# Kernel optimization log

Measured on AMD Instinct MI355X. Metric: run time of the kernel, lower is better.

## Reference

```python
import jax, jax.numpy as jnp
import numpy as np

WS = 14            # window height/width
CLS = 1            # cls tokens
DIM = 768
H = 12             # heads
DH = DIM // H      # head dim = 64
B = 128
N = WS * WS + CLS  # 197
SCALE = DH ** (-0.5)
TABLE = (2 * WS - 1) ** 2 + CLS  # 730


def _rel_index():
    # Swin-style relative position index, with CLS rows/cols pointing at the
    # last table entry (torch uses index -1 which wraps to TABLE-1).
    c = np.arange(WS)
    coords = np.stack(np.meshgrid(c, c, indexing='ij'))      # [2,14,14]
    cf = coords.reshape(2, -1)                                # [2,196]
    rel = cf[:, :, None] - cf[:, None, :]                     # [2,196,196]
    rel = rel.transpose(1, 2, 0).astype(np.int64)             # [196,196,2]
    rel[..., 0] += WS - 1
    rel[..., 1] += WS - 1
    rel[..., 0] *= 2 * WS - 1
    idx = rel.sum(-1)                                         # [196,196]
    full = np.full((N, N), -1, np.int64)
    full[CLS:, CLS:] = idx
    full = np.where(full < 0, TABLE - 1, full)
    return jnp.asarray(full, jnp.int32)


def setup_inputs() -> dict:
    key = jax.random.key(0)
    ks = jax.random.split(key, 5)
    return {
        'x': jax.random.normal(ks[0], (B, N, DIM), jnp.float32),
        'qkv_w': jax.random.normal(ks[1], (3 * DIM, DIM), jnp.float32) * 0.02,
        'proj_w': jax.random.normal(ks[2], (DIM, DIM), jnp.float32) * 0.02,
        'proj_b': jnp.zeros((DIM,), jnp.float32),
        'bias_table': jax.random.normal(ks[3], (TABLE, H), jnp.float32) * 0.02,
        'rel_idx': _rel_index(),
    }


def reference(x, qkv_w, proj_w, proj_b, bias_table, rel_idx):
    Bc, Nc, C = x.shape
    qkv = x @ qkv_w.T                                   # [B,N,3C]
    qkv = qkv.reshape(Bc, Nc, 3, H, DH).transpose(2, 0, 3, 1, 4)
    q, k, v = qkv[0], qkv[1], qkv[2]                    # [B,H,N,D]
    attn = jnp.einsum('bhnd,bhmd->bhnm', q, k) * SCALE  # [B,H,N,N]
    bias = bias_table[rel_idx]                          # [N,N,H]
    attn = attn + bias.transpose(2, 0, 1)[None]         # broadcast over batch
    attn = jax.nn.softmax(attn, axis=-1)
    out = jnp.einsum('bhnm,bhmd->bhnd', attn, v)        # [B,H,N,D]
    out = out.transpose(0, 2, 1, 3).reshape(Bc, Nc, C)
    return out @ proj_w.T + proj_b
```

## Files before the change

### kernel.cpp

```cpp
#include <hip/hip_runtime.h>
#include <hip/hip_bf16.h>

typedef _Float16 half8 __attribute__((ext_vector_type(8)));
typedef _Float16 half4 __attribute__((ext_vector_type(4)));
typedef float floatx4 __attribute__((ext_vector_type(4)));

#define MFMA16(a, b, c) __builtin_amdgcn_mfma_f32_16x16x32_f16(a, b, c, 0, 0, 0)
#define GLDS16(gp, lp) __builtin_amdgcn_global_load_lds( \
    (const __attribute__((address_space(1))) void*)(gp), \
    (__attribute__((address_space(3))) void*)(lp), 16, 0, 0)

#define BATCH 128
#define NTOK 197
#define NPAD 208
#define DIM 768
#define NH 12
#define DH 64
#define M_ROWS (BATCH * NTOK)
#define MP_ROWS (BATCH * NPAD)
#define KPAD 224
#define NKT 13
#define NTILES (BATCH * NH * NKT)

#define PREP_X (MP_ROWS * (DIM / 8))
#define PREP_WQ (3 * DIM * DIM / 8)
#define PREP_WP (DIM * DIM / 8)
#define PREP_B (NH * 13 * 13 * 256)
#define PREP_TOT (PREP_X + PREP_WQ + PREP_WP + PREP_B)

__device__ __forceinline__ half8 cvt8(const float* s) {
    float4 v0 = *(const float4*)s;
    float4 v1 = *(const float4*)(s + 4);
    half8 o;
    o[0] = (_Float16)v0.x; o[1] = (_Float16)v0.y;
    o[2] = (_Float16)v0.z; o[3] = (_Float16)v0.w;
    o[4] = (_Float16)v1.x; o[5] = (_Float16)v1.y;
    o[6] = (_Float16)v1.z; o[7] = (_Float16)v1.w;
    return o;
}

__global__ void prep_kernel(const float* __restrict__ x,
                            const float* __restrict__ qkv_w,
                            const float* __restrict__ proj_w,
                            const float* __restrict__ table,
                            const int* __restrict__ ridx,
                            _Float16* __restrict__ xh,
                            _Float16* __restrict__ wqkvh,
                            _Float16* __restrict__ wprojh,
                            _Float16* __restrict__ biasph) {
    int idx = blockIdx.x * 256 + threadIdx.x;
    if (idx < PREP_X) {
        int row = idx / (DIM / 8), ch = idx - row * (DIM / 8);
        int b = row / NPAD, n = row - b * NPAD;
        half8 o = {};
        if (n < NTOK) o = cvt8(x + (size_t)(b * NTOK + n) * DIM + ch * 8);
        *(half8*)&xh[(size_t)row * DIM + ch * 8] = o;
        return;
    }
    idx -= PREP_X;
    if (idx < PREP_WQ) {
        *(half8*)&wqkvh[idx * 8] = cvt8(qkv_w + idx * 8);
        return;
    }
    idx -= PREP_WQ;
    if (idx < PREP_WP) {
        *(half8*)&wprojh[idx * 8] = cvt8(proj_w + idx * 8);
        return;
    }
    idx -= PREP_WP;
    if (idx < PREP_B) {
        int e = idx & 255;
        int r = e >> 4, q = (e >> 2) & 3, rr = e & 3;
        int t = idx >> 8;
        int nt = t % 13; int t2 = t / 13; int qt = t2 % 13; int h = t2 / 13;
        int row = qt * 16 + q * 4 + rr;
        int col = nt * 16 + r;
        float v = -30000.0f;
        if (col < NTOK) {
            int rc = row < NTOK ? row : NTOK - 1;
            v = table[ridx[rc * NTOK + col] * NH + h];
        }
        biasph[idx] = (_Float16)v;
    }
}

__device__ __forceinline__ void gemm_core_768(const _Float16* __restrict__ A,
                                              const _Float16* __restrict__ B,
                                              int m0b, int n0b,
                                              _Float16* As, _Float16* Bs,
                                              floatx4 acc[4][4]) {
    const int lane = threadIdx.x & 63;
    const int w = threadIdx.x >> 6;
    const int r = lane & 15, q = lane >> 4;
    const int mo = (w & 1) * 64;
    const int no = (w >> 1) * 64;
    const int srow = w * 32 + (lane >> 3);
    const int gatom = (lane & 7) ^ (lane >> 3);
    const int rx = r & 7;

    const _Float16* pa[4];
    const _Float16* pb[4];
#pragma unroll
    for (int c = 0; c < 4; ++c) {
        pa[c] = A + (size_t)(m0b + srow + c * 8) * DIM + gatom * 8;
        pb[c] = B + (size_t)(n0b + srow + c * 8) * DIM + gatom * 8;
    }
    _Float16* ldsA = As + w * 2048;
    _Float16* ldsB = Bs + w * 2048;

    for (int kk = 0; kk < DIM / 64; ++kk) {
#pragma unroll
        for (int c = 0; c < 4; ++c) {
            GLDS16(pa[c], ldsA + c * 512);
            GLDS16(pb[c], ldsB + c * 512);
            pa[c] += 64;
            pb[c] += 64;
        }
        __syncthreads();
#pragma unroll
        for (int s = 0; s < 2; ++s) {
            half8 a[4], b[4];
#pragma unroll
            for (int i = 0; i < 4; ++i)
                a[i] = *(const half8*)&As[((mo + i * 16 + r) * 8 + ((s * 4 + q) ^ rx)) * 8];
#pragma unroll
            for (int j = 0; j < 4; ++j)
                b[j] = *(const half8*)&Bs[((no + j * 16 + r) * 8 + ((s * 4 + q) ^ rx)) * 8];
#pragma unroll
            for (int i = 0; i < 4; ++i)
#pragma unroll
                for (int j = 0; j < 4; ++j)
                    acc[i][j] = MFMA16(a[i], b[j], acc[i][j]);
        }
        __syncthreads();
    }
}

__global__ __launch_bounds__(256) void qkv_gemm(const _Float16* __restrict__ X,
                                                const _Float16* __restrict__ W,
                                                _Float16* __restrict__ qh,
                                                _Float16* __restrict__ kh,
                                                _Float16* __restrict__ vt) {
    __shared__ __align__(16) _Float16 smem[17408];
    _Float16* As = smem;
    _Float16* Bs = smem + 8192;
    const int lane = threadIdx.x & 63;
    const int w = threadIdx.x >> 6;
    const int r = lane & 15, q = lane >> 4;

    const int id = blockIdx.x;
    const int xcd = id & 7;
    const int lid = id >> 3;
    const int bx = lid % 18;
    const int by = xcd * 26 + lid / 18;
    const int m0b = by * 128;
    const int n0b = bx * 128;

    floatx4 acc[4][4] = {};
    gemm_core_768(X, W, m0b, n0b, As, Bs, acc);

    const int which = n0b / 768;
    const int gw = (w & 1) * 64;
    const int cw = (w >> 1) * 64;
    _Float16* T = smem;

    if (which == 2) {
#pragma unroll
        for (int i = 0; i < 4; ++i) {
#pragma unroll
            for (int j = 0; j < 4; ++j) {
                half4 hv;
#pragma unroll
                for (int rr = 0; rr < 4; ++rr) hv[rr] = (_Float16)acc[i][j][rr];
                *(half4*)&T[(cw + j * 16 + r) * 136 + gw + i * 16 + q * 4] = hv;
            }
        }
    } else {
        const float scale = (which == 0) ? 0.125f : 1.0f;
#pragma unroll
        for (int i = 0; i < 4; ++i)
#pragma unroll
            for (int j = 0; j < 4; ++j)
#pragma unroll
                for (int rr = 0; rr < 4; ++rr)
                    T[(gw + i * 16 + q * 4 + rr) * 136 + cw + j * 16 + r] =
                        (_Float16)(acc[i][j][rr] * scale);
    }
    __syncthreads();

    const int t = threadIdx.x;
    if (which == 2) {
#pragma unroll
        for (int p = 0; p < 8; ++p) {
            int idx = p * 256 + t;
            int c = idx >> 4, g0 = (idx & 15) * 8;
            int grow = m0b + g0;
            int b_idx = grow / NPAD, n_idx = grow - b_idx * NPAD;
            int vcol = n0b + c - 1536;
            int hh = vcol >> 6, d = vcol & 63;
            half8 hv = *(const half8*)&T[c * 136 + g0];
            *(half8*)&vt[((size_t)(b_idx * NH + hh) * DH + d) * KPAD + n_idx] = hv;
        }
    } else {
        _Float16* dst = (which == 0) ? qh : kh;
#pragma unroll
        for (int p = 0; p < 8; ++p) {
            int idx = p * 256 + t;
            int g = idx >> 4, c0 = (idx & 15) * 8;
            int grow = m0b + g;
            int b_idx = grow / NPAD, n_idx = grow - b_idx * NPAD;
            int colm = (n0b + c0) % 768;
            int hh = colm >> 6, d0 = colm & 63;
            half8 hv = *(const half8*)&T[g * 136 + c0];
            *(half8*)&dst[((size_t)(b_idx * NH + hh) * NPAD + n_idx) * DH + d0] = hv;
        }
    }
}

__global__ __launch_bounds__(256) void proj_gemm(const _Float16* __restrict__ A,
                                                 const _Float16* __restrict__ W,
                                                 const float* __restrict__ bias,
                                                 float* __restrict__ out) {
    __shared__ __align__(16) _Float16 As[128 * 64];
    __shared__ __align__(16) _Float16 Bs[128 * 64];
    const int lane = threadIdx.x & 63;
    const int w = threadIdx.x >> 6;
    const int r = lane & 15, q = lane >> 4;

    const int id = blockIdx.x;
    const int xcd = id & 7;
    const int lid = id >> 3;
    const int bx = lid % 6;
    const int by = xcd * 25 + lid / 6;
    if (by >= 197) return;
    const int m0b = by * 128;
    const int n0b = bx * 128;

    floatx4 acc[4][4] = {};
    gemm_core_768(A, W, m0b, n0b, As, Bs, acc);

    const int m0 = m0b + (w & 1) * 64;
    const int n0 = n0b + (w >> 1) * 64;
#pragma unroll
    for (int i = 0; i < 4; ++i) {
#pragma unroll
        for (int rr = 0; rr < 4; ++rr) {
            size_t grow = m0 + i * 16 + q * 4 + rr;
#pragma unroll
            for (int j = 0; j < 4; ++j) {
                int gcol = n0 + j * 16 + r;
                out[grow * DIM + gcol] = acc[i][j][rr] + bias[gcol];
            }
        }
    }
}

__global__ __launch_bounds__(256) void attn_kernel(const _Float16* __restrict__ qh,
                                                   const _Float16* __restrict__ kh,
                                                   const _Float16* __restrict__ vt,
                                                   const _Float16* __restrict__ biasph,
                                                   _Float16* __restrict__ ah) {
    __shared__ __align__(16) _Float16 P[4][16][40];
    const int w = threadIdx.x >> 6, lane = threadIdx.x & 63;
    const int r = lane & 15, q = lane >> 4;
    const int T = blockIdx.x * 4 + w;
    const int bh = T / 13;
    const int qt = T - bh * 13;
    const int b = bh / NH, h = bh - b * NH;
    const _Float16* Qb = qh + (size_t)bh * NPAD * DH;
    const _Float16* Kb = kh + (size_t)bh * NPAD * DH;
    const _Float16* Vtb = vt + (size_t)bh * DH * KPAD;

    half4 bf[NKT];
    const _Float16* bbase = biasph + (((size_t)h * 13 + qt) * 13) * 256 + r * 16 + q * 4;
#pragma unroll
    for (int nt = 0; nt < NKT; ++nt)
        bf[nt] = *(const half4*)(bbase + nt * 256);

    const int rowq = qt * 16 + r;
    half8 aq0 = *(const half8*)(Qb + (size_t)rowq * DH + q * 8);
    half8 aq1 = *(const half8*)(Qb + (size_t)rowq * DH + 32 + q * 8);

    floatx4 sacc[NKT] = {};
#pragma unroll
    for (int nt = 0; nt < NKT; ++nt) {
        int rowk = nt * 16 + r;
        half8 b0 = *(const half8*)(Kb + (size_t)rowk * DH + q * 8);
        half8 b1 = *(const half8*)(Kb + (size_t)rowk * DH + 32 + q * 8);
        sacc[nt] = MFMA16(aq0, b0, sacc[nt]);
        sacc[nt] = MFMA16(aq1, b1, sacc[nt]);
    }

    _Float16 pv[NKT][4];
#pragma unroll
    for (int rr = 0; rr < 4; ++rr) {
        float sv[NKT];
        float sm = 0.f;
#pragma unroll
        for (int nt = 0; nt < NKT; ++nt) {
            float e = __expf(sacc[nt][rr] + (float)bf[nt][rr]);
            sv[nt] = e;
            sm += e;
        }
#pragma unroll
        for (int m = 1; m <= 8; m <<= 1) sm += __shfl_xor(sm, m, 64);
        float inv = 1.0f / sm;
#pragma unroll
        for (int nt = 0; nt < NKT; ++nt)
            pv[nt][rr] = (_Float16)(sv[nt] * inv);
    }

    floatx4 oacc[4] = {};
    _Float16* Pw = &P[w][0][0];
#pragma unroll
    for (int kt = 0; kt < 7; ++kt) {
        const int nt0 = kt * 2, nt1 = kt * 2 + 1;
#pragma unroll
        for (int rr = 0; rr < 4; ++rr) {
            Pw[(q * 4 + rr) * 40 + r] = pv[nt0][rr];
            Pw[(q * 4 + rr) * 40 + 16 + r] = (nt1 < NKT) ? pv[nt1][rr] : (_Float16)0.0f;
        }
        __asm__ volatile("" ::: "memory");
        half8 ap = *(const half8*)&Pw[r * 40 + q * 8];
        __asm__ volatile("" ::: "memory");
#pragma unroll
        for (int dt = 0; dt < 4; ++dt) {
            half8 bv = *(const half8*)(Vtb + (size_t)(dt * 16 + r) * KPAD + kt * 32 + q * 8);
            oacc[dt] = MFMA16(ap, bv, oacc[dt]);
        }
    }

#pragma unroll
    for (int rr = 0; rr < 4; ++rr) {
        int row = qt * 16 + q * 4 + rr;
        if (row < NTOK) {
            size_t o = ((size_t)b * NTOK + row) * DIM + h * DH;
#pragma unroll
            for (int dt = 0; dt < 4; ++dt)
                ah[o + dt * 16 + r] = (_Float16)oacc[dt][rr];
        }
    }
}

extern "C" void kernel_launch(void* const* d_in, const int* in_sizes, int n_in,
                              void* d_out, int out_size, void* d_ws, size_t ws_size,
                              hipStream_t stream) {
    const float* x = (const float*)d_in[0];
    const float* qkv_w = (const float*)d_in[1];
    const float* proj_w = (const float*)d_in[2];
    const float* proj_b = (const float*)d_in[3];
    const float* table = (const float*)d_in[4];
    const int* ridx = (const int*)d_in[5];
    float* out = (float*)d_out;

    char* ws = (char*)d_ws;
    const size_t SZ_XP = (size_t)MP_ROWS * DIM * 2;
    const size_t SZ_WQKV = (size_t)3 * DIM * DIM * 2;
    const size_t SZ_WPROJ = (size_t)DIM * DIM * 2;
    const size_t SZ_QK = (size_t)BATCH * NH * NPAD * DH * 2;
    const size_t SZ_VT = (size_t)BATCH * NH * DH * KPAD * 2;
    const size_t SZ_BIAS = (size_t)NH * 13 * 13 * 256 * 2;

    _Float16* xh = (_Float16*)(ws + 0);
    _Float16* ah = (_Float16*)(ws + 0);
    _Float16* wqkvh = (_Float16*)(ws + SZ_XP);
    _Float16* wprojh = (_Float16*)(ws + SZ_XP + SZ_WQKV);
    _Float16* qh = (_Float16*)(ws + SZ_XP + SZ_WQKV + SZ_WPROJ);
    _Float16* kh = (_Float16*)(ws + SZ_XP + SZ_WQKV + SZ_WPROJ + SZ_QK);
    _Float16* vt = (_Float16*)(ws + SZ_XP + SZ_WQKV + SZ_WPROJ + 2 * SZ_QK);
    _Float16* biasph = (_Float16*)(ws + SZ_XP + SZ_WQKV + SZ_WPROJ + 2 * SZ_QK + SZ_VT);
    (void)SZ_BIAS; (void)ws_size; (void)n_in; (void)in_sizes; (void)out_size;

    prep_kernel<<<(PREP_TOT + 255) / 256, 256, 0, stream>>>(
        x, qkv_w, proj_w, table, ridx, xh, wqkvh, wprojh, biasph);
    qkv_gemm<<<3744, 256, 0, stream>>>(xh, wqkvh, qh, kh, vt);
    attn_kernel<<<NTILES / 4, 256, 0, stream>>>(qh, kh, vt, biasph, ah);
    proj_gemm<<<1200, 256, 0, stream>>>(ah, wprojh, proj_b, out);
}
```

Measured before the change: 427.3 us.

## Replace QKV GEMM with 256x256 eight-wave pipelined kernel using direct-to-LDS loads

The 128x128 four-wave QKV GEMM is replaced by a 256x256 tile kernel with 8 waves, double-buffered LDS filled through global_load_lds, and interleaved barriers with setprio around MFMA phases. The aim is to raise arithmetic intensity per tile and overlap global loads with MFMA work. The epilogue now writes each half-tile through LDS in turn. The attention kernel also gets an XCD-aware block remap for cache locality. The larger tile brings heavy register and LDS use and hand-written waitcnt/barrier logic that is fragile.

```diff
diff --git a/kernel.cpp b/kernel.cpp
--- a/kernel.cpp
+++ b/kernel.cpp
@@ -27,6 +27,14 @@
 #define PREP_WP (DIM * DIM / 8)
 #define PREP_B (NH * 13 * 13 * 256)
 #define PREP_TOT (PREP_X + PREP_WQ + PREP_WP + PREP_B)
+
+#define BAR() __asm__ volatile("s_barrier" ::: "memory")
+#define VMW4() __asm__ volatile("s_waitcnt vmcnt(4)" ::: "memory")
+#define VMW0() __asm__ volatile("s_waitcnt vmcnt(0)" ::: "memory")
+
+#define STG(gp, lp) do { \
+    GLDS16((gp), (lp)); \
+    GLDS16((gp) + 64 * DIM, (lp) + 4096); } while (0)
 
 __device__ __forceinline__ half8 cvt8(const float* s) {
     float4 v0 = *(const float4*)s;
@@ -84,6 +92,206 @@
     }
 }
 
+template <int VM, bool STA, bool STB>
+__device__ __forceinline__ void qkv_tile(int t, _Float16* smem,
+                                         const _Float16* ga0, const _Float16* ga1,
+                                         const _Float16* gb0, const _Float16* gb1,
+                                         int sbase, int r, int q, int wm, int wn,
+                                         floatx4 (&acc)[8][4]) {
+    const int buf = t & 1;
+    const int r7 = r & 7;
+    const int sl0 = (q ^ r7) * 8;
+    const int sl1 = sl0 ^ 32;
+    _Float16* base = smem + buf * 32768;
+    const _Float16* Ab = base + wm * 8192 + r * 64;
+    const _Float16* Bb = base + 16384 + (wn >> 1) * 8192 + ((wn & 1) * 64 + r) * 64;
+    _Float16* sA0 = smem + (buf ^ 1) * 32768 + sbase;
+    _Float16* sA1 = sA0 + 8192;
+    _Float16* sB0 = base + 16384 + sbase;
+    _Float16* sB1 = sB0 + 8192;
+    const int kof1 = (t + 1) * 64, kof2 = (t + 2) * 64;
+
+    half8 a[4][2], b[4][2];
+
+#pragma unroll
+    for (int i = 0; i < 4; ++i) {
+        a[i][0] = *(const half8*)(Ab + i * 1024 + sl0);
+        a[i][1] = *(const half8*)(Ab + i * 1024 + sl1);
+    }
+#pragma unroll
+    for (int j = 0; j < 2; ++j) {
+        b[j][0] = *(const half8*)(Bb + j * 1024 + sl0);
+        b[j][1] = *(const half8*)(Bb + j * 1024 + sl1);
+    }
+    if (STA) STG(ga0 + kof1, sA0);
+    BAR();
+    __builtin_amdgcn_s_setprio(1);
+#pragma unroll
+    for (int s = 0; s < 2; ++s)
+#pragma unroll
+        for (int i = 0; i < 4; ++i)
+#pragma unroll
+            for (int j = 0; j < 2; ++j)
+                acc[i][j] = MFMA16(a[i][s], b[j][s], acc[i][j]);
+    __builtin_amdgcn_s_setprio(0);
+    BAR();
+
+#pragma unroll
+    for (int j = 0; j < 2; ++j) {
+        b[2 + j][0] = *(const half8*)(Bb + (2 + j) * 1024 + sl0);
+        b[2 + j][1] = *(const half8*)(Bb + (2 + j) * 1024 + sl1);
+    }
+    if (STA) STG(ga1 + kof1, sA1);
+    BAR();
+    __builtin_amdgcn_s_setprio(1);
+#pragma unroll
+    for (int s = 0; s < 2; ++s)
+#pragma unroll
+        for (int i = 0; i < 4; ++i)
+#pragma unroll
+            for (int j = 0; j < 2; ++j)
+                acc[i][2 + j] = MFMA16(a[i][s], b[2 + j][s], acc[i][2 + j]);
+    __builtin_amdgcn_s_setprio(0);
+    BAR();
+
+#pragma unroll
+    for (int i = 0; i < 4; ++i) {
+        a[i][0] = *(const half8*)(Ab + (4 + i) * 1024 + sl0);
+        a[i][1] = *(const half8*)(Ab + (4 + i) * 1024 + sl1);
+    }
+    if (STB) STG(gb0 + kof2, sB0);
+    BAR();
+    __builtin_amdgcn_s_setprio(1);
+#pragma unroll
+    for (int s = 0; s < 2; ++s)
+#pragma unroll
+        for (int i = 0; i < 4; ++i)
+#pragma unroll
+            for (int j = 0; j < 2; ++j)
+                acc[4 + i][j] = MFMA16(a[i][s], b[j][s], acc[4 + i][j]);
+    __builtin_amdgcn_s_setprio(0);
+    BAR();
+
+    if (STB) STG(gb1 + kof2, sB1);
+    BAR();
+    __builtin_amdgcn_s_setprio(1);
+#pragma unroll
+    for (int s = 0; s < 2; ++s)
+#pragma unroll
+        for (int i = 0; i < 4; ++i)
+#pragma unroll
+            for (int j = 0; j < 2; ++j)
+                acc[4 + i][2 + j] = MFMA16(a[i][s], b[2 + j][s], acc[4 + i][2 + j]);
+    __builtin_amdgcn_s_setprio(0);
+    if (VM == 4) { VMW4(); }
+    else if (VM == 0) { VMW0(); }
+    BAR();
+}
+
+__global__ __launch_bounds__(512, 2) void qkv_gemm8(const _Float16* __restrict__ X,
+                                                    const _Float16* __restrict__ W,
+                                                    _Float16* __restrict__ qh,
+                                                    _Float16* __restrict__ kh,
+                                                    _Float16* __restrict__ vt) {
+    __shared__ __align__(16) _Float16 smem[65536];
+    const int tid = threadIdx.x;
+    const int lane = tid & 63, wid = tid >> 6;
+    const int r = lane & 15, q = lane >> 4;
+    const int wm = wid >> 2, wn = wid & 3;
+
+    const int id = blockIdx.x;
+    const int swz = (id & 7) * 117 + (id >> 3);
+    const int by = swz / 9, bx = swz - by * 9;
+    const int m0b = by * 256, n0b = bx * 256;
+
+    const int srow = wid * 8 + (lane >> 3);
+    const int sch = (lane & 7) ^ (lane >> 3);
+    const _Float16* ga0 = X + (size_t)(m0b + srow) * DIM + sch * 8;
+    const _Float16* ga1 = ga0 + (size_t)128 * DIM;
+    const _Float16* gb0 = W + (size_t)(n0b + srow) * DIM + sch * 8;
+    const _Float16* gb1 = gb0 + (size_t)128 * DIM;
+    const int sbase = wid * 512;
+
+    floatx4 acc[8][4] = {};
+
+    STG(ga0, smem + sbase);
+    STG(ga1, smem + 8192 + sbase);
+    STG(gb0, smem + 16384 + sbase);
+    STG(gb1, smem + 24576 + sbase);
+    STG(gb0 + 64, smem + 32768 + 16384 + sbase);
+    STG(gb1 + 64, smem + 32768 + 24576 + sbase);
+    VMW4();
+    BAR();
+
+#pragma unroll 2
+    for (int t = 0; t < 10; ++t)
+        qkv_tile<4, true, true>(t, smem, ga0, ga1, gb0, gb1, sbase, r, q, wm, wn, acc);
+    qkv_tile<0, true, false>(10, smem, ga0, ga1, gb0, gb1, sbase, r, q, wm, wn, acc);
+    qkv_tile<2, false, false>(11, smem, ga0, ga1, gb0, gb1, sbase, r, q, wm, wn, acc);
+
+    __syncthreads();
+    const int which = bx / 3;
+    const int cb = (bx - which * 3) * 256;
+    if (which == 2) {
+#pragma unroll
+        for (int hp = 0; hp < 2; ++hp) {
+            if (wm == hp) {
+#pragma unroll
+                for (int i = 0; i < 8; ++i)
+#pragma unroll
+                    for (int j = 0; j < 4; ++j) {
+                        half4 hv;
+#pragma unroll
+                        for (int rr = 0; rr < 4; ++rr) hv[rr] = (_Float16)acc[i][j][rr];
+                        *(half4*)&smem[(wn * 64 + j * 16 + r) * 136 + i * 16 + q * 4] = hv;
+                    }
+            }
+            __syncthreads();
+#pragma unroll
+            for (int p = 0; p < 8; ++p) {
+                int idx = p * 512 + tid;
+                int c = idx >> 4, g0 = (idx & 15) * 8;
+                int grow = m0b + hp * 128 + g0;
+                int b_idx = grow / NPAD, n_idx = grow - b_idx * NPAD;
+                int vcol = cb + c;
+                int hh = vcol >> 6, d = vcol & 63;
+                half8 hv = *(const half8*)&smem[c * 136 + g0];
+                *(half8*)&vt[((size_t)(b_idx * NH + hh) * DH + d) * KPAD + n_idx] = hv;
+            }
+            __syncthreads();
+        }
+    } else {
+        const float scale = (which == 0) ? 0.125f : 1.0f;
+        _Float16* dst = (which == 0) ? qh : kh;
+#pragma unroll
+        for (int hp = 0; hp < 2; ++hp) {
+            if (wm == hp) {
+#pragma unroll
+                for (int i = 0; i < 8; ++i)
+#pragma unroll
+                    for (int j = 0; j < 4; ++j)
+#pragma unroll
+                        for (int rr = 0; rr < 4; ++rr)
+                            smem[(i * 16 + q * 4 + rr) * 272 + wn * 64 + j * 16 + r] =
+                                (_Float16)(acc[i][j][rr] * scale);
+            }
+            __syncthreads();
+#pragma unroll
+            for (int p = 0; p < 8; ++p) {
+                int idx = p * 512 + tid;
+                int g = idx >> 5, c0 = (idx & 31) * 8;
+                int grow = m0b + hp * 128 + g;
+                int b_idx = grow / NPAD, n_idx = grow - b_idx * NPAD;
+                int colm = cb + c0;
+                int hh = colm >> 6, d0 = colm & 63;
+                half8 hv = *(const half8*)&smem[g * 272 + c0];
+                *(half8*)&dst[((size_t)(b_idx * NH + hh) * NPAD + n_idx) * DH + d0] = hv;
+            }
+            __syncthreads();
+        }
+    }
+}
+
 __device__ __forceinline__ void gemm_core_768(const _Float16* __restrict__ A,
                                               const _Float16* __restrict__ B,
                                               int m0b, int n0b,
@@ -136,87 +344,6 @@
     }
 }
 
-__global__ __launch_bounds__(256) void qkv_gemm(const _Float16* __restrict__ X,
-                                                const _Float16* __restrict__ W,
-                                                _Float16* __restrict__ qh,
-                                                _Float16* __restrict__ kh,
-                                                _Float16* __restrict__ vt) {
-    __shared__ __align__(16) _Float16 smem[17408];
-    _Float16* As = smem;
-    _Float16* Bs = smem + 8192;
-    const int lane = threadIdx.x & 63;
-    const int w = threadIdx.x >> 6;
-    const int r = lane & 15, q = lane >> 4;
-
-    const int id = blockIdx.x;
-    const int xcd = id & 7;
-    const int lid = id >> 3;
-    const int bx = lid % 18;
-    const int by = xcd * 26 + lid / 18;
-    const int m0b = by * 128;
-    const int n0b = bx * 128;
-
-    floatx4 acc[4][4] = {};
-    gemm_core_768(X, W, m0b, n0b, As, Bs, acc);
-
-    const int which = n0b / 768;
-    const int gw = (w & 1) * 64;
-    const int cw = (w >> 1) * 64;
-    _Float16* T = smem;
-
-    if (which == 2) {
-#pragma unroll
-        for (int i = 0; i < 4; ++i) {
-#pragma unroll
-            for (int j = 0; j < 4; ++j) {
-                half4 hv;
-#pragma unroll
-                for (int rr = 0; rr < 4; ++rr) hv[rr] = (_Float16)acc[i][j][rr];
-                *(half4*)&T[(cw + j * 16 + r) * 136 + gw + i * 16 + q * 4] = hv;
-            }
-        }
-    } else {
-        const float scale = (which == 0) ? 0.125f : 1.0f;
-#pragma unroll
-        for (int i = 0; i < 4; ++i)
-#pragma unroll
-            for (int j = 0; j < 4; ++j)
-#pragma unroll
-                for (int rr = 0; rr < 4; ++rr)
-                    T[(gw + i * 16 + q * 4 + rr) * 136 + cw + j * 16 + r] =
-                        (_Float16)(acc[i][j][rr] * scale);
-    }
-    __syncthreads();
-
-    const int t = threadIdx.x;
-    if (which == 2) {
-#pragma unroll
-        for (int p = 0; p < 8; ++p) {
-            int idx = p * 256 + t;
-            int c = idx >> 4, g0 = (idx & 15) * 8;
-            int grow = m0b + g0;
-            int b_idx = grow / NPAD, n_idx = grow - b_idx * NPAD;
-            int vcol = n0b + c - 1536;
-            int hh = vcol >> 6, d = vcol & 63;
-            half8 hv = *(const half8*)&T[c * 136 + g0];
-            *(half8*)&vt[((size_t)(b_idx * NH + hh) * DH + d) * KPAD + n_idx] = hv;
-        }
-    } else {
-        _Float16* dst = (which == 0) ? qh : kh;
-#pragma unroll
-        for (int p = 0; p < 8; ++p) {
-            int idx = p * 256 + t;
-            int g = idx >> 4, c0 = (idx & 15) * 8;
-            int grow = m0b + g;
-            int b_idx = grow / NPAD, n_idx = grow - b_idx * NPAD;
-            int colm = (n0b + c0) % 768;
-            int hh = colm >> 6, d0 = colm & 63;
-            half8 hv = *(const half8*)&T[g * 136 + c0];
-            *(half8*)&dst[((size_t)(b_idx * NH + hh) * NPAD + n_idx) * DH + d0] = hv;
-        }
-    }
-}
-
 __global__ __launch_bounds__(256) void proj_gemm(const _Float16* __restrict__ A,
                                                  const _Float16* __restrict__ W,
                                                  const float* __restrict__ bias,
@@ -263,7 +390,9 @@
     __shared__ __align__(16) _Float16 P[4][16][40];
     const int w = threadIdx.x >> 6, lane = threadIdx.x & 63;
     const int r = lane & 15, q = lane >> 4;
-    const int T = blockIdx.x * 4 + w;
+    const int id0 = blockIdx.x;
+    const int bid = (id0 & 7) * 624 + (id0 >> 3);
+    const int T = bid * 4 + w;
     const int bh = T / 13;
     const int qt = T - bh * 13;
     const int b = bh / NH, h = bh - b * NH;
@@ -373,7 +502,7 @@
 
     prep_kernel<<<(PREP_TOT + 255) / 256, 256, 0, stream>>>(
         x, qkv_w, proj_w, table, ridx, xh, wqkvh, wprojh, biasph);
-    qkv_gemm<<<3744, 256, 0, stream>>>(xh, wqkvh, qh, kh, vt);
+    qkv_gemm8<<<936, 512, 0, stream>>>(xh, wqkvh, qh, kh, vt);
     attn_kernel<<<NTILES / 4, 256, 0, stream>>>(qh, kh, vt, biasph, ah);
     proj_gemm<<<1200, 256, 0, stream>>>(ah, wprojh, proj_b, out);
 }
```

New measurement: 400.3 us. -6.3%, faster.
